# Kernel optimization log

Measured on AMD Instinct MI355X. Metric: run time of the kernel, lower is better.

## Reference

```python
import jax, jax.numpy as jnp
import numpy as np

EPS = 1e-8  # torch F.cosine_similarity eps
TEMP = 2.0  # hardcoded in module regardless of init arg


def _normalize(x):
    # row-normalize with torch-style eps clamp on the norm
    norm = jnp.sqrt(jnp.sum(x * x, axis=-1, keepdims=True))
    return x / jnp.maximum(norm, EPS)


def setup_inputs() -> dict:
    key = jax.random.key(0)
    k1, k2, k3 = jax.random.split(key, 3)
    n, m, d = 8192, 8192, 256
    return {
        "pos_key": jax.random.normal(k1, (n, d), dtype=jnp.float32),
        "pos_value": jax.random.normal(k2, (n, d), dtype=jnp.float32),
        "neg_value": jax.random.normal(k3, (m, d), dtype=jnp.float32),
    }


def reference(pos_key, pos_value, neg_value):
    pk = _normalize(pos_key)    # [n, d]
    pv = _normalize(pos_value)  # [n, d]
    nv = _normalize(neg_value)  # [m, d]

    pos_sim = jnp.sum(pk * pv, axis=-1)          # [n]
    neg_sim = jnp.einsum("nd,md->nm", pk, nv)    # [n, m] cosine sims

    pos_loss = -jnp.mean(pos_sim / TEMP)
    # log-sum-exp over m (stable), matching log(sum(exp(.)))
    neg_loss = jnp.mean(jax.scipy.special.logsumexp(neg_sim / TEMP, axis=-1))
    return pos_loss + neg_loss
```

## Files before the change

kernel.cpp:

```cpp
#include <hip/hip_runtime.h>

typedef __attribute__((ext_vector_type(4))) float f32x4;
typedef __attribute__((ext_vector_type(4))) int   i32x4;
typedef __attribute__((ext_vector_type(8))) int   i32x8;

#define DIM 256
#define D4  64

#define GLD_LDS16(g, l) __builtin_amdgcn_global_load_lds(                      \
    (const __attribute__((address_space(1))) void*)(g),                        \
    (__attribute__((address_space(3))) void*)(l), 16, 0, 0)

#define TILE_WAIT(N) asm volatile("s_waitcnt vmcnt(" #N ")\n\ts_barrier" ::: "memory")

__global__ __launch_bounds__(256) void normalize_kernel(
    const float4* __restrict__ pk, const float4* __restrict__ pv,
    const float4* __restrict__ nv, unsigned int* __restrict__ pkn,
    unsigned int* __restrict__ nvn, float* __restrict__ posPart, int N) {
  int row  = blockIdx.x * 4 + (threadIdx.x >> 6);
  int lane = threadIdx.x & 63;
  if (row < N) {
    float4 x = pk[row * D4 + lane];
    float4 y = pv[row * D4 + lane];
    float skk = x.x*x.x + x.y*x.y + x.z*x.z + x.w*x.w;
    float svv = y.x*y.x + y.y*y.y + y.z*y.z + y.w*y.w;
    float skv = x.x*y.x + x.y*y.y + x.z*y.z + x.w*y.w;
#pragma unroll
    for (int m = 32; m >= 1; m >>= 1) {
      skk += __shfl_xor(skk, m, 64);
      svv += __shfl_xor(svv, m, 64);
      skv += __shfl_xor(skv, m, 64);
    }
    float nk  = fmaxf(sqrtf(skk), 1e-8f);
    float nvv = fmaxf(sqrtf(svv), 1e-8f);
    if (lane == 0) posPart[row] = skv / (nk * nvv);
    float rk = 1.0f / nk;
    int w = __builtin_amdgcn_cvt_pk_fp8_f32(x.x * rk, x.y * rk, 0, false);
    w = __builtin_amdgcn_cvt_pk_fp8_f32(x.z * rk, x.w * rk, w, true);
    pkn[(size_t)row * 64 + lane] = (unsigned int)w;
  } else {
    int r2 = row - N;
    float4 x = nv[r2 * D4 + lane];
    float s = x.x*x.x + x.y*x.y + x.z*x.z + x.w*x.w;
#pragma unroll
    for (int m = 32; m >= 1; m >>= 1) s += __shfl_xor(s, m, 64);
    float rn = 1.0f / fmaxf(sqrtf(s), 1e-8f);
    int w = __builtin_amdgcn_cvt_pk_fp8_f32(x.x * rn, x.y * rn, 0, false);
    w = __builtin_amdgcn_cvt_pk_fp8_f32(x.z * rn, x.w * rn, w, true);
    nvn[(size_t)r2 * 64 + lane] = (unsigned int)w;
  }
}

__global__ __launch_bounds__(512, 2) void gemm_lse_kernel(
    const unsigned char* __restrict__ gA, const unsigned char* __restrict__ gB,
    float* __restrict__ partial, int N) {
  __shared__ unsigned char Bs[4][32768];

  const int tid  = threadIdx.x;
  const int lane = tid & 63;
  const int wv   = tid >> 6;
  const int wm   = wv >> 1;
  const int wn   = wv & 1;
  const int l15  = lane & 15, q = lane >> 4;
  const int cg    = blockIdx.x;
  const int panel = blockIdx.y;
  const int row0  = panel * 256;
  const int colBase = cg * 1024;
  const float kLog2eHalf = 0.72134752044448170f;
  const int kUnitScale = 0x7F7F7F7F;

  auto stageB = [&](int t) {
    const unsigned char* src = gB + (size_t)(colBase + t * 128) * 256;
    unsigned char* dst = &Bs[t & 3][0];
#pragma unroll
    for (int kb = 0; kb < 2; kb++)
#pragma unroll
      for (int i = 0; i < 2; i++) {
        int c  = i * 512 + tid;
        int r  = c >> 3;
        int sc = ((c & 7) ^ (r & 7)) << 4;
        GLD_LDS16(src + (size_t)r * 256 + kb * 128 + sc,
                  dst + kb * 16384 + c * 16);
      }
  };

  const unsigned char* aB = gA + (size_t)(row0 + wm * 64 + l15) * 256 + q * 32;
  i32x8 af[2][4];
#pragma unroll
  for (int kb = 0; kb < 2; kb++)
#pragma unroll
    for (int mi = 0; mi < 4; mi++)
      af[kb][mi] = *(const i32x8*)(aB + mi * 16 * 256 + kb * 128);
  __builtin_amdgcn_sched_barrier(0);

  stageB(0);
  stageB(1);
  stageB(2);
  __builtin_amdgcn_sched_barrier(0);

#pragma unroll
  for (int t = 0; t < 8; t++) {
    if      (t == 0) TILE_WAIT(7);
    else if (t == 1) TILE_WAIT(8);
    else if (t == 2) TILE_WAIT(9);
    else if (t == 3) TILE_WAIT(10);
    else if (t == 4) TILE_WAIT(10);
    else if (t == 5) TILE_WAIT(10);
    else if (t == 6) TILE_WAIT(6);
    else             TILE_WAIT(2);

    if (t < 5) {
      stageB(t + 3);
      __builtin_amdgcn_sched_barrier(0);
    }

    const unsigned char* bufB = &Bs[t & 3][0];
    f32x4 acc[4][4];
#pragma unroll
    for (int mi = 0; mi < 4; mi++)
#pragma unroll
      for (int ni = 0; ni < 4; ni++) acc[mi][ni] = (f32x4){0.f, 0.f, 0.f, 0.f};

#pragma unroll
    for (int kb = 0; kb < 2; kb++) {
      i32x8 bf[4];
#pragma unroll
      for (int ni = 0; ni < 4; ni++) {
        int r  = wn * 64 + ni * 16 + l15;
        int c0 = (q * 2)     ^ (r & 7);
        int c1 = (q * 2 + 1) ^ (r & 7);
        i32x4 lo = *(const i32x4*)(bufB + kb * 16384 + r * 128 + c0 * 16);
        i32x4 hi = *(const i32x4*)(bufB + kb * 16384 + r * 128 + c1 * 16);
        bf[ni] = (i32x8){lo.x, lo.y, lo.z, lo.w, hi.x, hi.y, hi.z, hi.w};
      }
#pragma unroll
      for (int mi = 0; mi < 4; mi++) {
        __builtin_amdgcn_s_setprio(1);
#pragma unroll
        for (int ni = 0; ni < 4; ni++)
          acc[mi][ni] = __builtin_amdgcn_mfma_scale_f32_16x16x128_f8f6f4(
              bf[ni], af[kb][mi], acc[mi][ni],
              0, 0, 0, kUnitScale, 0, kUnitScale);
        __builtin_amdgcn_s_setprio(0);
      }
    }

    float s0, s1, s2, s3;
#pragma unroll
    for (int mi = 0; mi < 4; mi++) {
      float v = 0.f;
#pragma unroll
      for (int ni = 0; ni < 4; ni++)
#pragma unroll
        for (int rr = 0; rr < 4; rr++)
          v += __builtin_amdgcn_exp2f(acc[mi][ni][rr] * kLog2eHalf);
      v += __shfl_xor(v, 16, 64);
      v += __shfl_xor(v, 32, 64);
      if (mi == 0) s0 = v; else if (mi == 1) s1 = v;
      else if (mi == 2) s2 = v; else s3 = v;
    }
    float o = q == 0 ? s0 : q == 1 ? s1 : q == 2 ? s2 : s3;
    int slab = cg * 16 + t * 2 + wn;
    partial[(size_t)slab * N + row0 + wm * 64 + q * 16 + l15] = o;
    __builtin_amdgcn_sched_barrier(0);
  }
}

__global__ __launch_bounds__(256) void finalize_kernel(
    const float* __restrict__ partial, const float* __restrict__ posPart,
    float* __restrict__ out, int N, int slabsPerGroup, float invN) {
  __shared__ float red[4][64];
  int t  = threadIdx.x;
  int rl = t & 63, g = t >> 6;
  int row = blockIdx.x * 64 + rl;
  const float* p = partial + (size_t)(g * slabsPerGroup) * N + row;
  float s = 0.f;
#pragma unroll 8
  for (int j = 0; j < slabsPerGroup; j++) s += p[(size_t)j * N];
  red[g][rl] = s;
  __syncthreads();
  if (t < 64) {
    float tot = red[0][rl] + red[1][rl] + red[2][rl] + red[3][rl];
    float v = __builtin_amdgcn_logf(tot) * 0.69314718055994531f
              - 0.5f * posPart[row];
#pragma unroll
    for (int m = 32; m >= 1; m >>= 1) v += __shfl_xor(v, m, 64);
    if (rl == 0) atomicAdd(out, v * invN);
  }
}

extern "C" void kernel_launch(void* const* d_in, const int* in_sizes, int n_in,
                              void* d_out, int out_size, void* d_ws, size_t ws_size,
                              hipStream_t stream) {
  const float* pk = (const float*)d_in[0];
  const float* pv = (const float*)d_in[1];
  const float* nv = (const float*)d_in[2];
  int N = in_sizes[0] / DIM;
  int M = in_sizes[2] / DIM;
  float* out = (float*)d_out;

  unsigned char* pkn = (unsigned char*)d_ws;
  unsigned char* nvn = pkn + (size_t)N * DIM;
  float* partial = (float*)(nvn + (size_t)M * DIM);
  float* posPart = partial + (size_t)(M / 64) * N;

  hipMemsetAsync(out, 0, sizeof(float), stream);

  normalize_kernel<<<(N + M) / 4, 256, 0, stream>>>(
      (const float4*)pk, (const float4*)pv, (const float4*)nv,
      (unsigned int*)pkn, (unsigned int*)nvn, posPart, N);

  gemm_lse_kernel<<<dim3(M / 1024, N / 256), 512, 0, stream>>>(
      pkn, nvn, partial, N);

  finalize_kernel<<<N / 64, 256, 0, stream>>>(
      partial, posPart, out, N, (M / 64) / 4, 1.0f / (float)N);
}
```

Baseline: 101.0 us.

## Fuse finalize reduction into GEMM via last-block counter and drop memset

```diff
diff --git a/kernel.cpp b/kernel.cpp
--- a/kernel.cpp
+++ b/kernel.cpp
@@ -16,7 +16,13 @@
 __global__ __launch_bounds__(256) void normalize_kernel(
     const float4* __restrict__ pk, const float4* __restrict__ pv,
     const float4* __restrict__ nv, unsigned int* __restrict__ pkn,
-    unsigned int* __restrict__ nvn, float* __restrict__ posPart, int N) {
+    unsigned int* __restrict__ nvn, float* __restrict__ posPart,
+    int* __restrict__ ctr, float* __restrict__ out, int N) {
+  if (blockIdx.x == 0) {
+    int t = threadIdx.x;
+    if (t < 32) ctr[t] = 0;
+    if (t == 32) out[0] = 0.f;
+  }
   int row  = blockIdx.x * 4 + (threadIdx.x >> 6);
   int lane = threadIdx.x & 63;
   if (row < N) {
@@ -53,8 +59,10 @@
 
 __global__ __launch_bounds__(512, 2) void gemm_lse_kernel(
     const unsigned char* __restrict__ gA, const unsigned char* __restrict__ gB,
-    float* __restrict__ partial, int N) {
+    float* __restrict__ partial, const float* __restrict__ posPart,
+    int* __restrict__ ctr, float* __restrict__ out, int N, float invN) {
   __shared__ unsigned char Bs[4][32768];
+  __shared__ int amLast;
 
   const int tid  = threadIdx.x;
   const int lane = tid & 63;
@@ -164,28 +172,32 @@
     partial[(size_t)slab * N + row0 + wm * 64 + q * 16 + l15] = o;
     __builtin_amdgcn_sched_barrier(0);
   }
-}
-
-__global__ __launch_bounds__(256) void finalize_kernel(
-    const float* __restrict__ partial, const float* __restrict__ posPart,
-    float* __restrict__ out, int N, int slabsPerGroup, float invN) {
-  __shared__ float red[4][64];
-  int t  = threadIdx.x;
-  int rl = t & 63, g = t >> 6;
-  int row = blockIdx.x * 64 + rl;
-  const float* p = partial + (size_t)(g * slabsPerGroup) * N + row;
-  float s = 0.f;
-#pragma unroll 8
-  for (int j = 0; j < slabsPerGroup; j++) s += p[(size_t)j * N];
-  red[g][rl] = s;
+
+  __threadfence();
   __syncthreads();
-  if (t < 64) {
-    float tot = red[0][rl] + red[1][rl] + red[2][rl] + red[3][rl];
-    float v = __builtin_amdgcn_logf(tot) * 0.69314718055994531f
-              - 0.5f * posPart[row];
-#pragma unroll
-    for (int m = 32; m >= 1; m >>= 1) v += __shfl_xor(v, m, 64);
-    if (rl == 0) atomicAdd(out, v * invN);
+  if (tid == 0) amLast = (atomicAdd(&ctr[panel], 1) == 7) ? 1 : 0;
+  __syncthreads();
+  if (amLast) {
+    __threadfence();
+    if (wv < 4) {
+      int row = row0 + wv * 64 + lane;
+      const float* p = partial + row;
+      float g0 = 0.f, g1 = 0.f, g2 = 0.f, g3 = 0.f;
+#pragma unroll 8
+      for (int j = 0; j < 32; j++) g0 += p[(size_t)j * N];
+#pragma unroll 8
+      for (int j = 0; j < 32; j++) g1 += p[(size_t)(32 + j) * N];
+#pragma unroll 8
+      for (int j = 0; j < 32; j++) g2 += p[(size_t)(64 + j) * N];
+#pragma unroll 8
+      for (int j = 0; j < 32; j++) g3 += p[(size_t)(96 + j) * N];
+      float tot = g0 + g1 + g2 + g3;
+      float v = __builtin_amdgcn_logf(tot) * 0.69314718055994531f
+                - 0.5f * posPart[row];
+#pragma unroll
+      for (int m = 32; m >= 1; m >>= 1) v += __shfl_xor(v, m, 64);
+      if (lane == 0) atomicAdd(out, v * invN);
+    }
   }
 }
 
@@ -203,16 +215,12 @@
   unsigned char* nvn = pkn + (size_t)N * DIM;
   float* partial = (float*)(nvn + (size_t)M * DIM);
   float* posPart = partial + (size_t)(M / 64) * N;
-
-  hipMemsetAsync(out, 0, sizeof(float), stream);
+  int*   ctr     = (int*)(posPart + N);
 
   normalize_kernel<<<(N + M) / 4, 256, 0, stream>>>(
       (const float4*)pk, (const float4*)pv, (const float4*)nv,
-      (unsigned int*)pkn, (unsigned int*)nvn, posPart, N);
+      (unsigned int*)pkn, (unsigned int*)nvn, posPart, ctr, out, N);
 
   gemm_lse_kernel<<<dim3(M / 1024, N / 256), 512, 0, stream>>>(
-      pkn, nvn, partial, N);
-
-  finalize_kernel<<<N / 64, 256, 0, stream>>>(
-      partial, posPart, out, N, (M / 64) / 4, 1.0f / (float)N);
+      pkn, nvn, partial, posPart, ctr, out, N, 1.0f / (float)N);
 }
```

Result: slower. 143.4 us (+41.9%).

## Load B fragments directly from global memory and fold output zeroing into normalize

Applied to the files above, without the earlier changes.

```diff
diff --git a/kernel.cpp b/kernel.cpp
--- a/kernel.cpp
+++ b/kernel.cpp
@@ -7,16 +7,12 @@
 #define DIM 256
 #define D4  64
 
-#define GLD_LDS16(g, l) __builtin_amdgcn_global_load_lds(                      \
-    (const __attribute__((address_space(1))) void*)(g),                        \
-    (__attribute__((address_space(3))) void*)(l), 16, 0, 0)
-
-#define TILE_WAIT(N) asm volatile("s_waitcnt vmcnt(" #N ")\n\ts_barrier" ::: "memory")
-
 __global__ __launch_bounds__(256) void normalize_kernel(
     const float4* __restrict__ pk, const float4* __restrict__ pv,
     const float4* __restrict__ nv, unsigned int* __restrict__ pkn,
-    unsigned int* __restrict__ nvn, float* __restrict__ posPart, int N) {
+    unsigned int* __restrict__ nvn, float* __restrict__ posPart,
+    float* __restrict__ out, int N) {
+  if (blockIdx.x == 0 && threadIdx.x == 0) out[0] = 0.f;
   int row  = blockIdx.x * 4 + (threadIdx.x >> 6);
   int lane = threadIdx.x & 63;
   if (row < N) {
@@ -54,8 +50,6 @@
 __global__ __launch_bounds__(512, 2) void gemm_lse_kernel(
     const unsigned char* __restrict__ gA, const unsigned char* __restrict__ gB,
     float* __restrict__ partial, int N) {
-  __shared__ unsigned char Bs[4][32768];
-
   const int tid  = threadIdx.x;
   const int lane = tid & 63;
   const int wv   = tid >> 6;
@@ -69,21 +63,6 @@
   const float kLog2eHalf = 0.72134752044448170f;
   const int kUnitScale = 0x7F7F7F7F;
 
-  auto stageB = [&](int t) {
-    const unsigned char* src = gB + (size_t)(colBase + t * 128) * 256;
-    unsigned char* dst = &Bs[t & 3][0];
-#pragma unroll
-    for (int kb = 0; kb < 2; kb++)
-#pragma unroll
-      for (int i = 0; i < 2; i++) {
-        int c  = i * 512 + tid;
-        int r  = c >> 3;
-        int sc = ((c & 7) ^ (r & 7)) << 4;
-        GLD_LDS16(src + (size_t)r * 256 + kb * 128 + sc,
-                  dst + kb * 16384 + c * 16);
-      }
-  };
-
   const unsigned char* aB = gA + (size_t)(row0 + wm * 64 + l15) * 256 + q * 32;
   i32x8 af[2][4];
 #pragma unroll
@@ -91,30 +70,18 @@
 #pragma unroll
     for (int mi = 0; mi < 4; mi++)
       af[kb][mi] = *(const i32x8*)(aB + mi * 16 * 256 + kb * 128);
-  __builtin_amdgcn_sched_barrier(0);
-
-  stageB(0);
-  stageB(1);
-  stageB(2);
-  __builtin_amdgcn_sched_barrier(0);
 
 #pragma unroll
   for (int t = 0; t < 8; t++) {
-    if      (t == 0) TILE_WAIT(7);
-    else if (t == 1) TILE_WAIT(8);
-    else if (t == 2) TILE_WAIT(9);
-    else if (t == 3) TILE_WAIT(10);
-    else if (t == 4) TILE_WAIT(10);
-    else if (t == 5) TILE_WAIT(10);
-    else if (t == 6) TILE_WAIT(6);
-    else             TILE_WAIT(2);
+    const unsigned char* bT =
+        gB + (size_t)(colBase + t * 128 + wn * 64 + l15) * 256 + q * 32;
+    i32x8 bf[2][4];
+#pragma unroll
+    for (int kb = 0; kb < 2; kb++)
+#pragma unroll
+      for (int ni = 0; ni < 4; ni++)
+        bf[kb][ni] = *(const i32x8*)(bT + ni * 16 * 256 + kb * 128);
 
-    if (t < 5) {
-      stageB(t + 3);
-      __builtin_amdgcn_sched_barrier(0);
-    }
-
-    const unsigned char* bufB = &Bs[t & 3][0];
     f32x4 acc[4][4];
 #pragma unroll
     for (int mi = 0; mi < 4; mi++)
@@ -122,28 +89,17 @@
       for (int ni = 0; ni < 4; ni++) acc[mi][ni] = (f32x4){0.f, 0.f, 0.f, 0.f};
 
 #pragma unroll
-    for (int kb = 0; kb < 2; kb++) {
-      i32x8 bf[4];
-#pragma unroll
-      for (int ni = 0; ni < 4; ni++) {
-        int r  = wn * 64 + ni * 16 + l15;
-        int c0 = (q * 2)     ^ (r & 7);
-        int c1 = (q * 2 + 1) ^ (r & 7);
-        i32x4 lo = *(const i32x4*)(bufB + kb * 16384 + r * 128 + c0 * 16);
-        i32x4 hi = *(const i32x4*)(bufB + kb * 16384 + r * 128 + c1 * 16);
-        bf[ni] = (i32x8){lo.x, lo.y, lo.z, lo.w, hi.x, hi.y, hi.z, hi.w};
-      }
+    for (int kb = 0; kb < 2; kb++)
 #pragma unroll
       for (int mi = 0; mi < 4; mi++) {
         __builtin_amdgcn_s_setprio(1);
 #pragma unroll
         for (int ni = 0; ni < 4; ni++)
           acc[mi][ni] = __builtin_amdgcn_mfma_scale_f32_16x16x128_f8f6f4(
-              bf[ni], af[kb][mi], acc[mi][ni],
+              bf[kb][ni], af[kb][mi], acc[mi][ni],
               0, 0, 0, kUnitScale, 0, kUnitScale);
         __builtin_amdgcn_s_setprio(0);
       }
-    }
 
     float s0, s1, s2, s3;
 #pragma unroll
@@ -162,7 +118,6 @@
     float o = q == 0 ? s0 : q == 1 ? s1 : q == 2 ? s2 : s3;
     int slab = cg * 16 + t * 2 + wn;
     partial[(size_t)slab * N + row0 + wm * 64 + q * 16 + l15] = o;
-    __builtin_amdgcn_sched_barrier(0);
   }
 }
 
@@ -204,11 +159,9 @@
   float* partial = (float*)(nvn + (size_t)M * DIM);
   float* posPart = partial + (size_t)(M / 64) * N;
 
-  hipMemsetAsync(out, 0, sizeof(float), stream);
-
   normalize_kernel<<<(N + M) / 4, 256, 0, stream>>>(
       (const float4*)pk, (const float4*)pv, (const float4*)nv,
-      (unsigned int*)pkn, (unsigned int*)nvn, posPart, N);
+      (unsigned int*)pkn, (unsigned int*)nvn, posPart, out, N);
 
   gemm_lse_kernel<<<dim3(M / 1024, N / 256), 512, 0, stream>>>(
       pkn, nvn, partial, N);
```

Measured after the change: 114.0 us. 1.13x slower.
